# Performance work log

Measured on AMD Instinct MI355X. Metric: run time of the kernel, lower is better.

Reference implementation:

```python
import jax, jax.numpy as jnp
import numpy as np

B, N, T, FD = 128, 64, 20, 2
E, H, A = 16, 32, 32
DB, DH = 30.0, 30.0
NB, NHD = 12, 12  # 360/30 bearing and heading bins
DOMAIN_INIT = 5.0
EPS = 1e-12


def setup_inputs() -> dict:
    key = jax.random.key(0)
    ks = jax.random.split(key, 20)
    rn = lambda k, s, sc=0.1: (jax.random.normal(k, s) * sc).astype(jnp.float32)
    return {
        'x': jax.random.normal(ks[0], (B, N, T, FD), jnp.float32),
        'dmat': jax.random.uniform(ks[1], (B, N, T, N), jnp.float32) * 10.0,
        'bmat': jax.random.uniform(ks[2], (B, N, T, N), jnp.float32) * 360.0,
        'hmat': jax.random.uniform(ks[3], (B, N, T, N), jnp.float32) * 360.0,
        'mask': jnp.ones((B, N, T), jnp.float32),
        'emb_W': rn(ks[4], (E, FD)), 'emb_b': rn(ks[5], (E,)),
        'W_ih': rn(ks[6], (4 * H, E)), 'W_hh': rn(ks[7], (4 * H, H)),
        'b_ih': rn(ks[8], (4 * H,)), 'b_hh': rn(ks[9], (4 * H,)),
        'domain': jnp.full((NB, NHD), DOMAIN_INIT, jnp.float32),
        'enc2att_W': rn(ks[10], (A, H)), 'enc2att_b': rn(ks[11], (A,)),
        'spa_W': rn(ks[12], (A, 2 * A)), 'spa_b': rn(ks[13], (A,)),
        'att2enc_W': rn(ks[14], (H, A)), 'att2enc_b': rn(ks[15], (H,)),
        'cls_W': rn(ks[16], (1, H)), 'cls_b': rn(ks[17], (1,)),
        'h0': jax.random.normal(ks[18], (B * N, H), jnp.float32),
        'c0': jax.random.normal(ks[19], (B * N, H), jnp.float32),
    }


def _forward(x, dmat, bmat, hmat, mask, emb_W, emb_b, W_ih, W_hh, b_ih, b_hh,
             domain, enc2att_W, enc2att_b, spa_W, spa_b, att2enc_W, att2enc_b,
             cls_W, cls_b, h0, c0):
    # input embedding: [B,N,T,F] -> [T, B*N, E] (time-major for scan)
    xe = jnp.einsum('bntf,ef->bnte', x, emb_W) + emb_b
    xe = jnp.moveaxis(xe.reshape(B * N, T, E), 1, 0)
    dm_t = jnp.moveaxis(dmat, 2, 0)   # [T,B,N,N]
    bm_t = jnp.moveaxis(bmat, 2, 0)
    hm_t = jnp.moveaxis(hmat, 2, 0)
    mk_t = jnp.moveaxis(mask, 2, 0)   # [T,B,N]
    eye = jnp.eye(N, dtype=x.dtype)

    def step(carry, inputs):
        h, c = carry                     # [B*N, H]
        xt, dm, bm, hm, mk = inputs
        # single-step LSTM cell (torch gate order i,f,g,o)
        g = xt @ W_ih.T + b_ih + h @ W_hh.T + b_hh
        i, f, gg, o = jnp.split(g, 4, axis=-1)
        c = jax.nn.sigmoid(f) * c + jax.nn.sigmoid(i) * jnp.tanh(gg)
        h = jax.nn.sigmoid(o) * jnp.tanh(c)
        # project encoder state to attention space: [B,N,A]
        a = h.reshape(B, N, H) @ enc2att_W.T + enc2att_b
        # spatial attention weights from distance/bearing/heading edge feats
        ib = jnp.clip(jnp.floor(bm / DB), 0, NB - 1).astype(jnp.int32)
        ih = jnp.clip(jnp.floor(hm / DH), 0, NHD - 1).astype(jnp.int32)
        w = jax.nn.relu(domain[ib, ih] - dm)               # [B,N,N]
        w = w * mk[:, :, None] * mk[:, None, :] * (1.0 - eye)
        w = w / (jnp.sum(w, axis=-1, keepdims=True) + EPS)
        att = jnp.einsum('bij,bjd->bid', w, a)
        z = jnp.tanh(jnp.concatenate([a, att], axis=-1) @ spa_W.T + spa_b)
        h = (z @ att2enc_W.T + att2enc_b).reshape(B * N, H)
        return (h, c), None

    (h, c), _ = jax.lax.scan(step, (h0, c0), (xe, dm_t, bm_t, hm_t, mk_t))
    scores = jnp.tanh(h.reshape(B, N, H) @ cls_W.T + cls_b)
    return jax.nn.sigmoid(scores)  # [B, N, 1]


def reference(x, dmat, bmat, hmat, mask, emb_W, emb_b, W_ih, W_hh, b_ih, b_hh,
              domain, enc2att_W, enc2att_b, spa_W, spa_b, att2enc_W, att2enc_b,
              cls_W, cls_b, h0, c0):
    return _forward(x, dmat, bmat, hmat, mask, emb_W, emb_b, W_ih, W_hh, b_ih,
                    b_hh, domain, enc2att_W, enc2att_b, spa_W, spa_b,
                    att2enc_W, att2enc_b, cls_W, cls_b, h0, c0)
```

## Files before the change

kernel.cpp:

```cpp
#include <hip/hip_runtime.h>
#include <math.h>

#define T_STEPS 20

typedef _Float16 half8 __attribute__((ext_vector_type(8)));
typedef _Float16 half4v __attribute__((ext_vector_type(4)));
typedef float f32x4 __attribute__((ext_vector_type(4)));

__device__ __forceinline__ float sigm(float v) {
  return __builtin_amdgcn_rcpf(1.0f + __expf(-v));
}
__device__ __forceinline__ float tanh_f(float v) {
  return 1.0f - 2.0f * __builtin_amdgcn_rcpf(1.0f + __expf(2.0f * v));
}

__global__ __launch_bounds__(1024)
void traj_disc(const float* __restrict__ x, const float* __restrict__ dmat,
               const float* __restrict__ bmat, const float* __restrict__ hmat,
               const float* __restrict__ maskp,
               const float* __restrict__ embW, const float* __restrict__ embb,
               const float* __restrict__ Wih, const float* __restrict__ Whh,
               const float* __restrict__ bih, const float* __restrict__ bhh,
               const float* __restrict__ dom,
               const float* __restrict__ e2aW, const float* __restrict__ e2ab,
               const float* __restrict__ spaW, const float* __restrict__ spab,
               const float* __restrict__ a2eW, const float* __restrict__ a2eb,
               const float* __restrict__ clsW, const float* __restrict__ clsb,
               const float* __restrict__ h0p, const float* __restrict__ c0p,
               float* __restrict__ out)
{
  __shared__ __align__(16) _Float16 sgw[128*40];
  __shared__ __align__(16) _Float16 sgwc[128*40];
  __shared__ __align__(16) float4   sgmb[128];
  __shared__ __align__(16) _Float16 sESaT[32*40];
  __shared__ __align__(16) _Float16 sEStT[32*40];
  __shared__ float bz[32];
  __shared__ float sdom[144];
  __shared__ float sm[1280];
  __shared__ float sclsc[32];
  __shared__ float sclsb2[1];
  __shared__ __align__(16) _Float16 sH[64*40];
  __shared__ __align__(16) _Float16 sw[64*72];
  __shared__ __align__(16) _Float16 sz_[64*40];
  __shared__ __align__(16) _Float16 sQT[32*72];
  __shared__ __align__(16) float sgates[128*68];

  const int tid = threadIdx.x;
  const int b = blockIdx.x;
  const int i = tid >> 4;
  const int s = tid & 15;
  const int w = tid >> 6;
  const int l = tid & 63;
  const int quad = l >> 4;
  const int n16 = l & 15;

  for (int idx = tid; idx < 4096; idx += 1024) sgw[(idx >> 5)*40 + (idx & 31)] = (_Float16)Whh[idx];
  {
    const int g = tid >> 3, kb = (tid & 7) << 2;
    float a0 = 0.f, a1 = 0.f, a2 = 0.f, a3 = 0.f;
    #pragma unroll
    for (int h = 0; h < 32; ++h) {
      const float wv = Whh[g*32 + h];
      a0 = fmaf(wv, a2eW[h*32 + kb + 0], a0);
      a1 = fmaf(wv, a2eW[h*32 + kb + 1], a1);
      a2 = fmaf(wv, a2eW[h*32 + kb + 2], a2);
      a3 = fmaf(wv, a2eW[h*32 + kb + 3], a3);
    }
    sgwc[g*40 + kb + 0] = (_Float16)a0; sgwc[g*40 + kb + 1] = (_Float16)a1;
    sgwc[g*40 + kb + 2] = (_Float16)a2; sgwc[g*40 + kb + 3] = (_Float16)a3;
  }
  if (tid < 128) {
    float m0 = 0.f, m1 = 0.f, b0 = bih[tid] + bhh[tid];
    #pragma unroll
    for (int e = 0; e < 16; ++e) {
      float wv_ = Wih[tid*16 + e];
      m0 = fmaf(wv_, embW[2*e],   m0);
      m1 = fmaf(wv_, embW[2*e+1], m1);
      b0 = fmaf(wv_, embb[e],     b0);
    }
    float bn = b0;
    #pragma unroll
    for (int h = 0; h < 32; ++h) bn = fmaf(Whh[tid*32 + h], a2eb[h], bn);
    sgmb[tid] = make_float4(m0, m1, b0, bn);
  }
  {
    const int zk = tid >> 5, hc = tid & 31;
    float sa_ = 0.f, st_ = 0.f;
    #pragma unroll
    for (int a = 0; a < 32; ++a) {
      const float ev = e2aW[a*32 + hc];
      sa_ = fmaf(spaW[zk*64 + a],      ev, sa_);
      st_ = fmaf(spaW[zk*64 + 32 + a], ev, st_);
    }
    sESaT[zk*40 + hc] = (_Float16)sa_;
    sEStT[zk*40 + hc] = (_Float16)st_;
  }
  if (tid < 32) {
    float acc = spab[tid];
    #pragma unroll
    for (int a = 0; a < 32; ++a)
      acc = fmaf(e2ab[a], spaW[tid*64 + a] + spaW[tid*64 + 32 + a], acc);
    bz[tid] = acc;
    float cc = 0.f;
    #pragma unroll
    for (int h = 0; h < 32; ++h) cc = fmaf(clsW[h], a2eW[h*32 + tid], cc);
    sclsc[tid] = cc;
  }
  if (tid == 0) {
    float cb = clsb[0];
    #pragma unroll
    for (int h = 0; h < 32; ++h) cb = fmaf(clsW[h], a2eb[h], cb);
    sclsb2[0] = cb;
  }
  if (tid < 144) sdom[tid] = dom[tid];
  for (int idx = tid; idx < 1280; idx += 1024) sm[idx] = maskp[(size_t)b*1280 + idx];
  for (int idx = tid; idx < 2048; idx += 1024) sH[(idx >> 5)*40 + (idx & 31)] = (_Float16)h0p[(size_t)b*2048 + idx];
  float c0r = c0p[(size_t)b*2048 + i*32 + s];
  float c1r = c0p[(size_t)b*2048 + i*32 + s + 16];
  __syncthreads();

  const size_t nb = (size_t)b*64 + i;

  const float* xpre = x + (size_t)(b*64 + ((w >> 2) << 4) + (quad << 2)) * 40;
  float2 xA = *(const float2*)(xpre +   0);
  float2 xB = *(const float2*)(xpre +  40);
  float2 xC = *(const float2*)(xpre +  80);
  float2 xD = *(const float2*)(xpre + 120);
  size_t eb_ = nb*1280;
  float dm0 = dmat[eb_ + s],      bm0 = bmat[eb_ + s],      hm0 = hmat[eb_ + s];
  float dm1 = dmat[eb_ + s + 16], bm1 = bmat[eb_ + s + 16], hm1 = hmat[eb_ + s + 16];
  float dm2 = dmat[eb_ + s + 32], bm2 = bmat[eb_ + s + 32], hm2 = hmat[eb_ + s + 32];
  float dm3 = dmat[eb_ + s + 48], bm3 = bmat[eb_ + s + 48], hm3 = hmat[eb_ + s + 48];

  #pragma unroll 1
  for (int t = 0; t < T_STEPS; ++t) {
    {
      const int r1 = w >> 2, cp = (w & 3) << 1;
      const _Float16* Abase = (t == 0) ? sH : sz_;
      const _Float16* Bbase = (t == 0) ? sgw : sgwc;
      const half8 Af = *(const half8*)(Abase + (16*r1 + n16)*40 + quad*8);
#define OP1C(c) { \
      const half8 Bf = *(const half8*)(Bbase + (16*(c) + n16)*40 + quad*8); \
      const float4 mb = sgmb[16*(c) + n16]; \
      const float bb = (t == 0) ? mb.z : mb.w; \
      f32x4 Cv; \
      Cv[0] = fmaf(xA.x, mb.x, fmaf(xA.y, mb.y, bb)); \
      Cv[1] = fmaf(xB.x, mb.x, fmaf(xB.y, mb.y, bb)); \
      Cv[2] = fmaf(xC.x, mb.x, fmaf(xC.y, mb.y, bb)); \
      Cv[3] = fmaf(xD.x, mb.x, fmaf(xD.y, mb.y, bb)); \
      Cv = __builtin_amdgcn_mfma_f32_16x16x32_f16(Af, Bf, Cv, 0, 0, 0); \
      *(f32x4*)(sgates + (16*(c) + n16)*68 + 16*r1 + 4*quad) = Cv; }
      OP1C(cp) OP1C(cp + 1)
#undef OP1C
    }
    __syncthreads();

    {
#define GR(q, u) sgates[((q)*32 + s + 16*(u))*68 + i]
      const float ai0 = GR(0,0), af0 = GR(1,0), ag0 = GR(2,0), ao0 = GR(3,0);
      const float ai1 = GR(0,1), af1 = GR(1,1), ag1 = GR(2,1), ao1 = GR(3,1);
#undef GR
      c0r = fmaf(sigm(af0), c0r, sigm(ai0)*tanh_f(ag0));
      sH[i*40 + s]      = (_Float16)(sigm(ao0)*tanh_f(c0r));
      c1r = fmaf(sigm(af1), c1r, sigm(ai1)*tanh_f(ag1));
      sH[i*40 + s + 16] = (_Float16)(sigm(ao1)*tanh_f(c1r));
    }
    {
      const float mi_ = sm[i*20 + t];
      float rs = 0.0f;
#define WCOMP(jj) float wn##jj; { \
      int ib_ = (int)floorf(bm##jj * (1.0f/30.0f)); ib_ = ib_ < 0 ? 0 : (ib_ > 11 ? 11 : ib_); \
      int ih_ = (int)floorf(hm##jj * (1.0f/30.0f)); ih_ = ih_ < 0 ? 0 : (ih_ > 11 ? 11 : ih_); \
      float w_ = fmaxf(sdom[ib_*12 + ih_] - dm##jj, 0.0f) * (mi_ * sm[(s + 16*(jj))*20 + t]); \
      wn##jj = (s + 16*(jj) == i) ? 0.0f : w_; rs += wn##jj; }
      WCOMP(0) WCOMP(1) WCOMP(2) WCOMP(3)
#undef WCOMP
      rs += __shfl_xor(rs, 1); rs += __shfl_xor(rs, 2);
      rs += __shfl_xor(rs, 4); rs += __shfl_xor(rs, 8);
      const float inv_ = __builtin_amdgcn_rcpf(rs + 1e-12f);
      sw[i*72 + s +  0] = (_Float16)(wn0 * inv_);
      sw[i*72 + s + 16] = (_Float16)(wn1 * inv_);
      sw[i*72 + s + 32] = (_Float16)(wn2 * inv_);
      sw[i*72 + s + 48] = (_Float16)(wn3 * inv_);
    }
    {
      const int tn = (t < T_STEPS - 1) ? t + 1 : t;
      const size_t ebn = (nb*20 + tn)*64;
      dm0 = dmat[ebn + s];      bm0 = bmat[ebn + s];      hm0 = hmat[ebn + s];
      dm1 = dmat[ebn + s + 16]; bm1 = bmat[ebn + s + 16]; hm1 = hmat[ebn + s + 16];
      dm2 = dmat[ebn + s + 32]; bm2 = bmat[ebn + s + 32]; hm2 = hmat[ebn + s + 32];
      dm3 = dmat[ebn + s + 48]; bm3 = bmat[ebn + s + 48]; hm3 = hmat[ebn + s + 48];
      const int tn2 = tn << 1;
      xA = *(const float2*)(xpre + tn2);
      xB = *(const float2*)(xpre + tn2 +  40);
      xC = *(const float2*)(xpre + tn2 +  80);
      xD = *(const float2*)(xpre + tn2 + 120);
    }
    __syncthreads();

    f32x4 Pv = {0.f, 0.f, 0.f, 0.f};
    if (w < 8) {
      const int r = w >> 1, c = w & 1;
      const half8 Af = *(const half8*)(sH    + (16*r + n16)*40 + quad*8);
      const half8 Bf = *(const half8*)(sESaT + (16*c + n16)*40 + quad*8);
      const float bzv = bz[16*c + n16];
      Pv[0] = bzv; Pv[1] = bzv; Pv[2] = bzv; Pv[3] = bzv;
      Pv = __builtin_amdgcn_mfma_f32_16x16x32_f16(Af, Bf, Pv, 0, 0, 0);
    } else {
      const int w8 = w - 8, r = w8 >> 1, c = w8 & 1;
      const half8 Af = *(const half8*)(sH    + (16*r + n16)*40 + quad*8);
      const half8 Bf = *(const half8*)(sEStT + (16*c + n16)*40 + quad*8);
      f32x4 Cv = {0.f, 0.f, 0.f, 0.f};
      Cv = __builtin_amdgcn_mfma_f32_16x16x32_f16(Af, Bf, Cv, 0, 0, 0);
      half4v hq;
      hq[0] = (_Float16)Cv[0]; hq[1] = (_Float16)Cv[1];
      hq[2] = (_Float16)Cv[2]; hq[3] = (_Float16)Cv[3];
      *(half4v*)(sQT + (16*c + n16)*72 + 16*r + 4*quad) = hq;
    }
    __syncthreads();

    if (w < 8) {
      const int r = w >> 1, c = w & 1;
      const half8 A0 = *(const half8*)(sw  + (16*r + n16)*72 + quad*8);
      const half8 A1 = *(const half8*)(sw  + (16*r + n16)*72 + 32 + quad*8);
      const half8 B0 = *(const half8*)(sQT + (16*c + n16)*72 + quad*8);
      const half8 B1 = *(const half8*)(sQT + (16*c + n16)*72 + 32 + quad*8);
      Pv = __builtin_amdgcn_mfma_f32_16x16x32_f16(A0, B0, Pv, 0, 0, 0);
      Pv = __builtin_amdgcn_mfma_f32_16x16x32_f16(A1, B1, Pv, 0, 0, 0);
      const int nd = 16*r + 4*quad;
      sz_[(nd+0)*40 + 16*c + n16] = (_Float16)tanh_f(Pv[0]);
      sz_[(nd+1)*40 + 16*c + n16] = (_Float16)tanh_f(Pv[1]);
      sz_[(nd+2)*40 + 16*c + n16] = (_Float16)tanh_f(Pv[2]);
      sz_[(nd+3)*40 + 16*c + n16] = (_Float16)tanh_f(Pv[3]);
    }
    __syncthreads();
  }

  if (tid < 64) {
    float acc = sclsb2[0];
    #pragma unroll
    for (int k = 0; k < 32; ++k) acc = fmaf((float)sz_[tid*40 + k], sclsc[k], acc);
    out[(size_t)b*64 + tid] = sigm(tanh_f(acc));
  }
}

extern "C" void kernel_launch(void* const* d_in, const int* in_sizes, int n_in,
                              void* d_out, int out_size, void* d_ws, size_t ws_size,
                              hipStream_t stream) {
  (void)in_sizes; (void)n_in; (void)d_ws; (void)ws_size; (void)out_size;
  const float* x    = (const float*)d_in[0];
  const float* dmat = (const float*)d_in[1];
  const float* bmat = (const float*)d_in[2];
  const float* hmat = (const float*)d_in[3];
  const float* mask = (const float*)d_in[4];
  const float* embW = (const float*)d_in[5];
  const float* embb = (const float*)d_in[6];
  const float* Wih  = (const float*)d_in[7];
  const float* Whh  = (const float*)d_in[8];
  const float* bih  = (const float*)d_in[9];
  const float* bhh  = (const float*)d_in[10];
  const float* dom  = (const float*)d_in[11];
  const float* e2aW = (const float*)d_in[12];
  const float* e2ab = (const float*)d_in[13];
  const float* spaW = (const float*)d_in[14];
  const float* spab = (const float*)d_in[15];
  const float* a2eW = (const float*)d_in[16];
  const float* a2eb = (const float*)d_in[17];
  const float* clsW = (const float*)d_in[18];
  const float* clsb = (const float*)d_in[19];
  const float* h0   = (const float*)d_in[20];
  const float* c0   = (const float*)d_in[21];
  float* out = (float*)d_out;

  traj_disc<<<dim3(128), dim3(1024), 0, stream>>>(
      x, dmat, bmat, hmat, mask, embW, embb, Wih, Whh, bih, bhh, dom,
      e2aW, e2ab, spaW, spab, a2eW, a2eb, clsW, clsb, h0, c0, out);
}
```

Measured before the change: 225.0 us.

## Specialize waves into LSTM and attention-weight groups and drop two barriers per step

Waves 0-7 now compute all eight gate tiles for their row block, apply the LSTM nonlinearities directly on the MFMA accumulators, and recompute the full Q projection each. Waves 8-15 take over the edge-weight computation and the dmat/bmat/hmat prefetch, with 8 edges per thread. This removes the sgates LDS round trip and cuts the barriers per timestep from four to two. The cost is that each of waves 0-7 repeats the Q MFMA work, several waves write identical sQT values, and register pressure per thread goes up.

After: 239.9 us. 1.07x slower.

```diff
diff --git a/kernel.cpp b/kernel.cpp
--- a/kernel.cpp
+++ b/kernel.cpp
@@ -4,7 +4,6 @@
 #define T_STEPS 20
 
 typedef _Float16 half8 __attribute__((ext_vector_type(8)));
-typedef _Float16 half4v __attribute__((ext_vector_type(4)));
 typedef float f32x4 __attribute__((ext_vector_type(4)));
 
 __device__ __forceinline__ float sigm(float v) {
@@ -40,15 +39,12 @@
   __shared__ float sclsc[32];
   __shared__ float sclsb2[1];
   __shared__ __align__(16) _Float16 sH[64*40];
-  __shared__ __align__(16) _Float16 sw[64*72];
+  __shared__ __align__(16) _Float16 sw_[64*72];
   __shared__ __align__(16) _Float16 sz_[64*40];
   __shared__ __align__(16) _Float16 sQT[32*72];
-  __shared__ __align__(16) float sgates[128*68];
 
   const int tid = threadIdx.x;
   const int b = blockIdx.x;
-  const int i = tid >> 4;
-  const int s = tid & 15;
   const int w = tid >> 6;
   const int l = tid & 63;
   const int quad = l >> 4;
@@ -115,32 +111,57 @@
   if (tid < 144) sdom[tid] = dom[tid];
   for (int idx = tid; idx < 1280; idx += 1024) sm[idx] = maskp[(size_t)b*1280 + idx];
   for (int idx = tid; idx < 2048; idx += 1024) sH[(idx >> 5)*40 + (idx & 31)] = (_Float16)h0p[(size_t)b*2048 + idx];
-  float c0r = c0p[(size_t)b*2048 + i*32 + s];
-  float c1r = c0p[(size_t)b*2048 + i*32 + s + 16];
   __syncthreads();
 
-  const size_t nb = (size_t)b*64 + i;
-
-  const float* xpre = x + (size_t)(b*64 + ((w >> 2) << 4) + (quad << 2)) * 40;
-  float2 xA = *(const float2*)(xpre +   0);
-  float2 xB = *(const float2*)(xpre +  40);
-  float2 xC = *(const float2*)(xpre +  80);
-  float2 xD = *(const float2*)(xpre + 120);
-  size_t eb_ = nb*1280;
-  float dm0 = dmat[eb_ + s],      bm0 = bmat[eb_ + s],      hm0 = hmat[eb_ + s];
-  float dm1 = dmat[eb_ + s + 16], bm1 = bmat[eb_ + s + 16], hm1 = hmat[eb_ + s + 16];
-  float dm2 = dmat[eb_ + s + 32], bm2 = bmat[eb_ + s + 32], hm2 = hmat[eb_ + s + 32];
-  float dm3 = dmat[eb_ + s + 48], bm3 = bmat[eb_ + s + 48], hm3 = hmat[eb_ + s + 48];
+  int r = 0, csel = 0;
+  half8 EA = {0}, ET = {0};
+  float bzv = 0.f;
+  const float* xpre = x;
+  float2 xA = {0,0}, xB = {0,0}, xC = {0,0}, xD = {0,0};
+  float cA0=0, cA1=0, cA2=0, cA3=0, cB0=0, cB1=0, cB2=0, cB3=0;
+  int i3 = 0, s8 = 0;
+  float dm0=0,dm1=0,dm2=0,dm3=0,dm4=0,dm5=0,dm6=0,dm7=0;
+  float bm0=0,bm1=0,bm2=0,bm3=0,bm4=0,bm5=0,bm6=0,bm7=0;
+  float hm0=0,hm1=0,hm2=0,hm3=0,hm4=0,hm5=0,hm6=0,hm7=0;
+
+  if (w < 8) {
+    r = w >> 1; csel = w & 1;
+    EA = *(const half8*)(sESaT + (16*csel + n16)*40 + quad*8);
+    ET = *(const half8*)(sEStT + (16*csel + n16)*40 + quad*8);
+    bzv = bz[16*csel + n16];
+    xpre = x + (size_t)(b*64 + 16*r + 4*quad) * 40;
+    xA = *(const float2*)(xpre +   0);
+    xB = *(const float2*)(xpre +  40);
+    xC = *(const float2*)(xpre +  80);
+    xD = *(const float2*)(xpre + 120);
+    const size_t cb0 = (size_t)(b*64 + 16*r + 4*quad)*32 + n16;
+    cA0 = c0p[cb0];        cA1 = c0p[cb0 + 32];
+    cA2 = c0p[cb0 + 64];   cA3 = c0p[cb0 + 96];
+    cB0 = c0p[cb0 + 16];   cB1 = c0p[cb0 + 48];
+    cB2 = c0p[cb0 + 80];   cB3 = c0p[cb0 + 112];
+  } else {
+    const int t8 = tid - 512;
+    i3 = t8 >> 3; s8 = t8 & 7;
+    const size_t eb0 = ((size_t)(b*64 + i3)*20 + 0)*64 + s8;
+    dm0 = dmat[eb0];      bm0 = bmat[eb0];      hm0 = hmat[eb0];
+    dm1 = dmat[eb0 +  8]; bm1 = bmat[eb0 +  8]; hm1 = hmat[eb0 +  8];
+    dm2 = dmat[eb0 + 16]; bm2 = bmat[eb0 + 16]; hm2 = hmat[eb0 + 16];
+    dm3 = dmat[eb0 + 24]; bm3 = bmat[eb0 + 24]; hm3 = hmat[eb0 + 24];
+    dm4 = dmat[eb0 + 32]; bm4 = bmat[eb0 + 32]; hm4 = hmat[eb0 + 32];
+    dm5 = dmat[eb0 + 40]; bm5 = bmat[eb0 + 40]; hm5 = hmat[eb0 + 40];
+    dm6 = dmat[eb0 + 48]; bm6 = bmat[eb0 + 48]; hm6 = hmat[eb0 + 48];
+    dm7 = dmat[eb0 + 56]; bm7 = bmat[eb0 + 56]; hm7 = hmat[eb0 + 56];
+  }
 
   #pragma unroll 1
   for (int t = 0; t < T_STEPS; ++t) {
-    {
-      const int r1 = w >> 2, cp = (w & 3) << 1;
-      const _Float16* Abase = (t == 0) ? sH : sz_;
-      const _Float16* Bbase = (t == 0) ? sgw : sgwc;
-      const half8 Af = *(const half8*)(Abase + (16*r1 + n16)*40 + quad*8);
-#define OP1C(c) { \
-      const half8 Bf = *(const half8*)(Bbase + (16*(c) + n16)*40 + quad*8); \
+    if (w < 8) {
+      const _Float16* Ab = (t == 0) ? sH : sz_;
+      const _Float16* Bb = (t == 0) ? sgw : sgwc;
+      const half8 Af = *(const half8*)(Ab + (16*r + n16)*40 + quad*8);
+      f32x4 G0, G1, G2, G3, G4, G5, G6, G7;
+#define OP1C(c, Gd) { \
+      const half8 Bf = *(const half8*)(Bb + (16*(c) + n16)*40 + quad*8); \
       const float4 mb = sgmb[16*(c) + n16]; \
       const float bb = (t == 0) ? mb.z : mb.w; \
       f32x4 Cv; \
@@ -148,90 +169,86 @@
       Cv[1] = fmaf(xB.x, mb.x, fmaf(xB.y, mb.y, bb)); \
       Cv[2] = fmaf(xC.x, mb.x, fmaf(xC.y, mb.y, bb)); \
       Cv[3] = fmaf(xD.x, mb.x, fmaf(xD.y, mb.y, bb)); \
-      Cv = __builtin_amdgcn_mfma_f32_16x16x32_f16(Af, Bf, Cv, 0, 0, 0); \
-      *(f32x4*)(sgates + (16*(c) + n16)*68 + 16*r1 + 4*quad) = Cv; }
-      OP1C(cp) OP1C(cp + 1)
+      Gd = __builtin_amdgcn_mfma_f32_16x16x32_f16(Af, Bf, Cv, 0, 0, 0); }
+      OP1C(0, G0) OP1C(1, G1) OP1C(2, G2) OP1C(3, G3)
+      OP1C(4, G4) OP1C(5, G5) OP1C(6, G6) OP1C(7, G7)
 #undef OP1C
-    }
-    __syncthreads();
-
-    {
-#define GR(q, u) sgates[((q)*32 + s + 16*(u))*68 + i]
-      const float ai0 = GR(0,0), af0 = GR(1,0), ag0 = GR(2,0), ao0 = GR(3,0);
-      const float ai1 = GR(0,1), af1 = GR(1,1), ag1 = GR(2,1), ao1 = GR(3,1);
-#undef GR
-      c0r = fmaf(sigm(af0), c0r, sigm(ai0)*tanh_f(ag0));
-      sH[i*40 + s]      = (_Float16)(sigm(ao0)*tanh_f(c0r));
-      c1r = fmaf(sigm(af1), c1r, sigm(ai1)*tanh_f(ag1));
-      sH[i*40 + s + 16] = (_Float16)(sigm(ao1)*tanh_f(c1r));
-    }
-    {
-      const float mi_ = sm[i*20 + t];
+#define NL(Gi, Gf, Gg, Go, k, creg, hho) { \
+      const float ii = sigm(Gi[k]), ff = sigm(Gf[k]); \
+      const float gg = tanh_f(Gg[k]), oo = sigm(Go[k]); \
+      creg = fmaf(ff, creg, ii*gg); \
+      sH[(16*r + 4*quad + (k))*40 + n16 + (hho)] = (_Float16)(oo * tanh_f(creg)); }
+      NL(G0, G2, G4, G6, 0, cA0, 0)  NL(G0, G2, G4, G6, 1, cA1, 0)
+      NL(G0, G2, G4, G6, 2, cA2, 0)  NL(G0, G2, G4, G6, 3, cA3, 0)
+      NL(G1, G3, G5, G7, 0, cB0, 16) NL(G1, G3, G5, G7, 1, cB1, 16)
+      NL(G1, G3, G5, G7, 2, cB2, 16) NL(G1, G3, G5, G7, 3, cB3, 16)
+#undef NL
+    } else {
+      const float mi_ = sm[i3*20 + t];
       float rs = 0.0f;
 #define WCOMP(jj) float wn##jj; { \
       int ib_ = (int)floorf(bm##jj * (1.0f/30.0f)); ib_ = ib_ < 0 ? 0 : (ib_ > 11 ? 11 : ib_); \
       int ih_ = (int)floorf(hm##jj * (1.0f/30.0f)); ih_ = ih_ < 0 ? 0 : (ih_ > 11 ? 11 : ih_); \
-      float w_ = fmaxf(sdom[ib_*12 + ih_] - dm##jj, 0.0f) * (mi_ * sm[(s + 16*(jj))*20 + t]); \
-      wn##jj = (s + 16*(jj) == i) ? 0.0f : w_; rs += wn##jj; }
-      WCOMP(0) WCOMP(1) WCOMP(2) WCOMP(3)
+      float w_ = fmaxf(sdom[ib_*12 + ih_] - dm##jj, 0.0f) * (mi_ * sm[(s8 + 8*(jj))*20 + t]); \
+      wn##jj = (s8 + 8*(jj) == i3) ? 0.0f : w_; rs += wn##jj; }
+      WCOMP(0) WCOMP(1) WCOMP(2) WCOMP(3) WCOMP(4) WCOMP(5) WCOMP(6) WCOMP(7)
 #undef WCOMP
-      rs += __shfl_xor(rs, 1); rs += __shfl_xor(rs, 2);
-      rs += __shfl_xor(rs, 4); rs += __shfl_xor(rs, 8);
+      rs += __shfl_xor(rs, 1); rs += __shfl_xor(rs, 2); rs += __shfl_xor(rs, 4);
       const float inv_ = __builtin_amdgcn_rcpf(rs + 1e-12f);
-      sw[i*72 + s +  0] = (_Float16)(wn0 * inv_);
-      sw[i*72 + s + 16] = (_Float16)(wn1 * inv_);
-      sw[i*72 + s + 32] = (_Float16)(wn2 * inv_);
-      sw[i*72 + s + 48] = (_Float16)(wn3 * inv_);
-    }
-    {
-      const int tn = (t < T_STEPS - 1) ? t + 1 : t;
-      const size_t ebn = (nb*20 + tn)*64;
-      dm0 = dmat[ebn + s];      bm0 = bmat[ebn + s];      hm0 = hmat[ebn + s];
-      dm1 = dmat[ebn + s + 16]; bm1 = bmat[ebn + s + 16]; hm1 = hmat[ebn + s + 16];
-      dm2 = dmat[ebn + s + 32]; bm2 = bmat[ebn + s + 32]; hm2 = hmat[ebn + s + 32];
-      dm3 = dmat[ebn + s + 48]; bm3 = bmat[ebn + s + 48]; hm3 = hmat[ebn + s + 48];
-      const int tn2 = tn << 1;
+      sw_[i3*72 + s8 +  0] = (_Float16)(wn0 * inv_);
+      sw_[i3*72 + s8 +  8] = (_Float16)(wn1 * inv_);
+      sw_[i3*72 + s8 + 16] = (_Float16)(wn2 * inv_);
+      sw_[i3*72 + s8 + 24] = (_Float16)(wn3 * inv_);
+      sw_[i3*72 + s8 + 32] = (_Float16)(wn4 * inv_);
+      sw_[i3*72 + s8 + 40] = (_Float16)(wn5 * inv_);
+      sw_[i3*72 + s8 + 48] = (_Float16)(wn6 * inv_);
+      sw_[i3*72 + s8 + 56] = (_Float16)(wn7 * inv_);
+    }
+    __syncthreads();
+
+    if (w < 8) {
+      const half8 Hr0 = *(const half8*)(sH + (      n16)*40 + quad*8);
+      const half8 Hr1 = *(const half8*)(sH + (16  + n16)*40 + quad*8);
+      const half8 Hr2 = *(const half8*)(sH + (32  + n16)*40 + quad*8);
+      const half8 Hr3 = *(const half8*)(sH + (48  + n16)*40 + quad*8);
+      const half8 HrR = (r == 0) ? Hr0 : (r == 1) ? Hr1 : (r == 2) ? Hr2 : Hr3;
+      f32x4 Pv = {bzv, bzv, bzv, bzv};
+      Pv = __builtin_amdgcn_mfma_f32_16x16x32_f16(HrR, EA, Pv, 0, 0, 0);
+#define QT(rq, Afr) { \
+      f32x4 Qv = {0.f, 0.f, 0.f, 0.f}; \
+      Qv = __builtin_amdgcn_mfma_f32_16x16x32_f16(Afr, ET, Qv, 0, 0, 0); \
+      _Float16* qd = sQT + (16*csel + n16)*72 + 16*(rq) + 4*quad; \
+      qd[0] = (_Float16)Qv[0]; qd[1] = (_Float16)Qv[1]; \
+      qd[2] = (_Float16)Qv[2]; qd[3] = (_Float16)Qv[3]; }
+      QT(0, Hr0) QT(1, Hr1) QT(2, Hr2) QT(3, Hr3)
+#undef QT
+      const half8 A0 = *(const half8*)(sw_ + (16*r + n16)*72 + quad*8);
+      const half8 A1 = *(const half8*)(sw_ + (16*r + n16)*72 + 32 + quad*8);
+      const half8 B0 = *(const half8*)(sQT + (16*csel + n16)*72 + quad*8);
+      const half8 B1 = *(const half8*)(sQT + (16*csel + n16)*72 + 32 + quad*8);
+      Pv = __builtin_amdgcn_mfma_f32_16x16x32_f16(A0, B0, Pv, 0, 0, 0);
+      Pv = __builtin_amdgcn_mfma_f32_16x16x32_f16(A1, B1, Pv, 0, 0, 0);
+      _Float16* zd = sz_ + (16*r + 4*quad)*40 + 16*csel + n16;
+      zd[0]   = (_Float16)tanh_f(Pv[0]);
+      zd[40]  = (_Float16)tanh_f(Pv[1]);
+      zd[80]  = (_Float16)tanh_f(Pv[2]);
+      zd[120] = (_Float16)tanh_f(Pv[3]);
+      const int tn2 = ((t < T_STEPS - 1) ? t + 1 : t) << 1;
       xA = *(const float2*)(xpre + tn2);
       xB = *(const float2*)(xpre + tn2 +  40);
       xC = *(const float2*)(xpre + tn2 +  80);
       xD = *(const float2*)(xpre + tn2 + 120);
-    }
-    __syncthreads();
-
-    f32x4 Pv = {0.f, 0.f, 0.f, 0.f};
-    if (w < 8) {
-      const int r = w >> 1, c = w & 1;
-      const half8 Af = *(const half8*)(sH    + (16*r + n16)*40 + quad*8);
-      const half8 Bf = *(const half8*)(sESaT + (16*c + n16)*40 + quad*8);
-      const float bzv = bz[16*c + n16];
-      Pv[0] = bzv; Pv[1] = bzv; Pv[2] = bzv; Pv[3] = bzv;
-      Pv = __builtin_amdgcn_mfma_f32_16x16x32_f16(Af, Bf, Pv, 0, 0, 0);
     } else {
-      const int w8 = w - 8, r = w8 >> 1, c = w8 & 1;
-      const half8 Af = *(const half8*)(sH    + (16*r + n16)*40 + quad*8);
-      const half8 Bf = *(const half8*)(sEStT + (16*c + n16)*40 + quad*8);
-      f32x4 Cv = {0.f, 0.f, 0.f, 0.f};
-      Cv = __builtin_amdgcn_mfma_f32_16x16x32_f16(Af, Bf, Cv, 0, 0, 0);
-      half4v hq;
-      hq[0] = (_Float16)Cv[0]; hq[1] = (_Float16)Cv[1];
-      hq[2] = (_Float16)Cv[2]; hq[3] = (_Float16)Cv[3];
-      *(half4v*)(sQT + (16*c + n16)*72 + 16*r + 4*quad) = hq;
-    }
-    __syncthreads();
-
-    if (w < 8) {
-      const int r = w >> 1, c = w & 1;
-      const half8 A0 = *(const half8*)(sw  + (16*r + n16)*72 + quad*8);
-      const half8 A1 = *(const half8*)(sw  + (16*r + n16)*72 + 32 + quad*8);
-      const half8 B0 = *(const half8*)(sQT + (16*c + n16)*72 + quad*8);
-      const half8 B1 = *(const half8*)(sQT + (16*c + n16)*72 + 32 + quad*8);
-      Pv = __builtin_amdgcn_mfma_f32_16x16x32_f16(A0, B0, Pv, 0, 0, 0);
-      Pv = __builtin_amdgcn_mfma_f32_16x16x32_f16(A1, B1, Pv, 0, 0, 0);
-      const int nd = 16*r + 4*quad;
-      sz_[(nd+0)*40 + 16*c + n16] = (_Float16)tanh_f(Pv[0]);
-      sz_[(nd+1)*40 + 16*c + n16] = (_Float16)tanh_f(Pv[1]);
-      sz_[(nd+2)*40 + 16*c + n16] = (_Float16)tanh_f(Pv[2]);
-      sz_[(nd+3)*40 + 16*c + n16] = (_Float16)tanh_f(Pv[3]);
+      const int tn = (t < T_STEPS - 1) ? t + 1 : t;
+      const size_t ebn = ((size_t)(b*64 + i3)*20 + tn)*64 + s8;
+      dm0 = dmat[ebn];      bm0 = bmat[ebn];      hm0 = hmat[ebn];
+      dm1 = dmat[ebn +  8]; bm1 = bmat[ebn +  8]; hm1 = hmat[ebn +  8];
+      dm2 = dmat[ebn + 16]; bm2 = bmat[ebn + 16]; hm2 = hmat[ebn + 16];
+      dm3 = dmat[ebn + 24]; bm3 = bmat[ebn + 24]; hm3 = hmat[ebn + 24];
+      dm4 = dmat[ebn + 32]; bm4 = bmat[ebn + 32]; hm4 = hmat[ebn + 32];
+      dm5 = dmat[ebn + 40]; bm5 = bmat[ebn + 40]; hm5 = hmat[ebn + 40];
+      dm6 = dmat[ebn + 48]; bm6 = bmat[ebn + 48]; hm6 = hmat[ebn + 48];
+      dm7 = dmat[ebn + 56]; bm7 = bmat[ebn + 56]; hm7 = hmat[ebn + 56];
     }
     __syncthreads();
   }
```

## Precompute normalized attention weights in a parallel prep kernel before recurrence

Applied to the files above, without the earlier changes.

Moves the per-timestep edge-weight computation (domain lookup, relu, masking, row normalization) out of the serial 20-step recurrence into a separate fully parallel kernel that writes fp16 weights to workspace. The main kernel then loads the weight fragments straight into MFMA operand registers, prefetching the next step's fragments. It also hoists the constant spatial-projection B fragments into registers. This takes the weight math off the critical path and drops one sync per step, at the cost of an extra launch and an fp16 round-trip through global memory. A fallback path keeps the old fused kernel when the workspace is too small.

After: 238.0 us. 5.8% more time.

```diff
diff --git a/kernel.cpp b/kernel.cpp
--- a/kernel.cpp
+++ b/kernel.cpp
@@ -14,20 +14,270 @@
   return 1.0f - 2.0f * __builtin_amdgcn_rcpf(1.0f + __expf(2.0f * v));
 }
 
+__global__ __launch_bounds__(256)
+void prep_w(const float* __restrict__ dmat, const float* __restrict__ bmat,
+            const float* __restrict__ hmat, const float* __restrict__ maskp,
+            const float* __restrict__ dom, _Float16* __restrict__ wout)
+{
+  __shared__ float sdom[144];
+  __shared__ float smk[64];
+  const int tid = threadIdx.x;
+  const int bt = blockIdx.x;
+  const int b = bt / 20, t = bt - b*20;
+  if (tid < 144) sdom[tid] = dom[tid];
+  if (tid < 64) smk[tid] = maskp[(size_t)b*1280 + tid*20 + t];
+  __syncthreads();
+  const int i  = tid >> 2;
+  const int jb = (tid & 3) << 4;
+  const size_t eb = ((size_t)(b*64 + i)*20 + t)*64 + jb;
+  const float mi = smk[i];
+  float rs = 0.f;
+#define WC(k) float wv##k; { \
+  const float dmv = dmat[eb + (k)]; \
+  const float bmv = bmat[eb + (k)]; \
+  const float hmv = hmat[eb + (k)]; \
+  int ib_ = (int)floorf(bmv * (1.0f/30.0f)); ib_ = ib_ < 0 ? 0 : (ib_ > 11 ? 11 : ib_); \
+  int ih_ = (int)floorf(hmv * (1.0f/30.0f)); ih_ = ih_ < 0 ? 0 : (ih_ > 11 ? 11 : ih_); \
+  float w_ = fmaxf(sdom[ib_*12 + ih_] - dmv, 0.0f) * (mi * smk[jb + (k)]); \
+  wv##k = (jb + (k) == i) ? 0.0f : w_; rs += wv##k; }
+  WC(0) WC(1) WC(2) WC(3) WC(4) WC(5) WC(6) WC(7)
+  WC(8) WC(9) WC(10) WC(11) WC(12) WC(13) WC(14) WC(15)
+#undef WC
+  rs += __shfl_xor(rs, 1); rs += __shfl_xor(rs, 2);
+  const float inv = __builtin_amdgcn_rcpf(rs + 1e-12f);
+  half8 o0, o1;
+  o0[0]=(_Float16)(wv0*inv);  o0[1]=(_Float16)(wv1*inv);
+  o0[2]=(_Float16)(wv2*inv);  o0[3]=(_Float16)(wv3*inv);
+  o0[4]=(_Float16)(wv4*inv);  o0[5]=(_Float16)(wv5*inv);
+  o0[6]=(_Float16)(wv6*inv);  o0[7]=(_Float16)(wv7*inv);
+  o1[0]=(_Float16)(wv8*inv);  o1[1]=(_Float16)(wv9*inv);
+  o1[2]=(_Float16)(wv10*inv); o1[3]=(_Float16)(wv11*inv);
+  o1[4]=(_Float16)(wv12*inv); o1[5]=(_Float16)(wv13*inv);
+  o1[6]=(_Float16)(wv14*inv); o1[7]=(_Float16)(wv15*inv);
+  _Float16* dst = wout + ((size_t)bt*64 + i)*64 + jb;
+  *(half8*)(dst)     = o0;
+  *(half8*)(dst + 8) = o1;
+}
+
 __global__ __launch_bounds__(1024)
-void traj_disc(const float* __restrict__ x, const float* __restrict__ dmat,
-               const float* __restrict__ bmat, const float* __restrict__ hmat,
-               const float* __restrict__ maskp,
-               const float* __restrict__ embW, const float* __restrict__ embb,
-               const float* __restrict__ Wih, const float* __restrict__ Whh,
-               const float* __restrict__ bih, const float* __restrict__ bhh,
-               const float* __restrict__ dom,
-               const float* __restrict__ e2aW, const float* __restrict__ e2ab,
-               const float* __restrict__ spaW, const float* __restrict__ spab,
-               const float* __restrict__ a2eW, const float* __restrict__ a2eb,
-               const float* __restrict__ clsW, const float* __restrict__ clsb,
-               const float* __restrict__ h0p, const float* __restrict__ c0p,
-               float* __restrict__ out)
+void traj_disc_main(const float* __restrict__ x,
+                    const float* __restrict__ embW, const float* __restrict__ embb,
+                    const float* __restrict__ Wih, const float* __restrict__ Whh,
+                    const float* __restrict__ bih, const float* __restrict__ bhh,
+                    const float* __restrict__ e2aW, const float* __restrict__ e2ab,
+                    const float* __restrict__ spaW, const float* __restrict__ spab,
+                    const float* __restrict__ a2eW, const float* __restrict__ a2eb,
+                    const float* __restrict__ clsW, const float* __restrict__ clsb,
+                    const float* __restrict__ h0p, const float* __restrict__ c0p,
+                    const _Float16* __restrict__ wglob,
+                    float* __restrict__ out)
+{
+  __shared__ __align__(16) _Float16 sgw[128*40];
+  __shared__ __align__(16) _Float16 sgwc[128*40];
+  __shared__ __align__(16) float4   sgmb[128];
+  __shared__ __align__(16) _Float16 sESaT[32*40];
+  __shared__ __align__(16) _Float16 sEStT[32*40];
+  __shared__ float bz[32];
+  __shared__ float sclsc[32];
+  __shared__ float sclsb2[1];
+  __shared__ __align__(16) _Float16 sH[64*40];
+  __shared__ __align__(16) _Float16 sz_[64*40];
+  __shared__ __align__(16) _Float16 sQT[32*72];
+  __shared__ __align__(16) float sgates[128*68];
+
+  const int tid = threadIdx.x;
+  const int b = blockIdx.x;
+  const int i = tid >> 4;
+  const int s = tid & 15;
+  const int w = tid >> 6;
+  const int l = tid & 63;
+  const int quad = l >> 4;
+  const int n16 = l & 15;
+
+  for (int idx = tid; idx < 4096; idx += 1024) sgw[(idx >> 5)*40 + (idx & 31)] = (_Float16)Whh[idx];
+  {
+    const int g = tid >> 3, kb = (tid & 7) << 2;
+    float a0 = 0.f, a1 = 0.f, a2 = 0.f, a3 = 0.f;
+    #pragma unroll
+    for (int h = 0; h < 32; ++h) {
+      const float wv = Whh[g*32 + h];
+      a0 = fmaf(wv, a2eW[h*32 + kb + 0], a0);
+      a1 = fmaf(wv, a2eW[h*32 + kb + 1], a1);
+      a2 = fmaf(wv, a2eW[h*32 + kb + 2], a2);
+      a3 = fmaf(wv, a2eW[h*32 + kb + 3], a3);
+    }
+    sgwc[g*40 + kb + 0] = (_Float16)a0; sgwc[g*40 + kb + 1] = (_Float16)a1;
+    sgwc[g*40 + kb + 2] = (_Float16)a2; sgwc[g*40 + kb + 3] = (_Float16)a3;
+  }
+  if (tid < 128) {
+    float m0 = 0.f, m1 = 0.f, b0 = bih[tid] + bhh[tid];
+    #pragma unroll
+    for (int e = 0; e < 16; ++e) {
+      float wv_ = Wih[tid*16 + e];
+      m0 = fmaf(wv_, embW[2*e],   m0);
+      m1 = fmaf(wv_, embW[2*e+1], m1);
+      b0 = fmaf(wv_, embb[e],     b0);
+    }
+    float bn = b0;
+    #pragma unroll
+    for (int h = 0; h < 32; ++h) bn = fmaf(Whh[tid*32 + h], a2eb[h], bn);
+    sgmb[tid] = make_float4(m0, m1, b0, bn);
+  }
+  {
+    const int zk = tid >> 5, hc = tid & 31;
+    float sa_ = 0.f, st_ = 0.f;
+    #pragma unroll
+    for (int a = 0; a < 32; ++a) {
+      const float ev = e2aW[a*32 + hc];
+      sa_ = fmaf(spaW[zk*64 + a],      ev, sa_);
+      st_ = fmaf(spaW[zk*64 + 32 + a], ev, st_);
+    }
+    sESaT[zk*40 + hc] = (_Float16)sa_;
+    sEStT[zk*40 + hc] = (_Float16)st_;
+  }
+  if (tid < 32) {
+    float acc = spab[tid];
+    #pragma unroll
+    for (int a = 0; a < 32; ++a)
+      acc = fmaf(e2ab[a], spaW[tid*64 + a] + spaW[tid*64 + 32 + a], acc);
+    bz[tid] = acc;
+    float cc = 0.f;
+    #pragma unroll
+    for (int h = 0; h < 32; ++h) cc = fmaf(clsW[h], a2eW[h*32 + tid], cc);
+    sclsc[tid] = cc;
+  }
+  if (tid == 0) {
+    float cb = clsb[0];
+    #pragma unroll
+    for (int h = 0; h < 32; ++h) cb = fmaf(clsW[h], a2eb[h], cb);
+    sclsb2[0] = cb;
+  }
+  for (int idx = tid; idx < 2048; idx += 1024) sH[(idx >> 5)*40 + (idx & 31)] = (_Float16)h0p[(size_t)b*2048 + idx];
+  float c0r = c0p[(size_t)b*2048 + i*32 + s];
+  float c1r = c0p[(size_t)b*2048 + i*32 + s + 16];
+  __syncthreads();
+
+  const float* xpre = x + (size_t)(b*64 + ((w >> 2) << 4) + (quad << 2)) * 40;
+  float2 xA = *(const float2*)(xpre +   0);
+  float2 xB = *(const float2*)(xpre +  40);
+  float2 xC = *(const float2*)(xpre +  80);
+  float2 xD = *(const float2*)(xpre + 120);
+  half8 Bconst;
+  float bzv = 0.f;
+  half8 wA0 = {0}, wA1 = {0};
+  if (w < 8) {
+    const int c = w & 1, r = w >> 1;
+    Bconst = *(const half8*)(sESaT + (16*c + n16)*40 + quad*8);
+    bzv = bz[16*c + n16];
+    const _Float16* wp = wglob + ((size_t)(b*20 + 0)*64 + 16*r + n16)*64 + quad*8;
+    wA0 = *(const half8*)(wp);
+    wA1 = *(const half8*)(wp + 32);
+  } else {
+    const int c = (w - 8) & 1;
+    Bconst = *(const half8*)(sEStT + (16*c + n16)*40 + quad*8);
+  }
+
+  #pragma unroll 1
+  for (int t = 0; t < T_STEPS; ++t) {
+    {
+      const int r1 = w >> 2, cp = (w & 3) << 1;
+      const _Float16* Ab = (t == 0) ? sH : sz_;
+      const _Float16* Bb = (t == 0) ? sgw : sgwc;
+      const half8 Af = *(const half8*)(Ab + (16*r1 + n16)*40 + quad*8);
+#define OP1C(c) { \
+      const half8 Bf = *(const half8*)(Bb + (16*(c) + n16)*40 + quad*8); \
+      const float4 mb = sgmb[16*(c) + n16]; \
+      const float bb = (t == 0) ? mb.z : mb.w; \
+      f32x4 Cv; \
+      Cv[0] = fmaf(xA.x, mb.x, fmaf(xA.y, mb.y, bb)); \
+      Cv[1] = fmaf(xB.x, mb.x, fmaf(xB.y, mb.y, bb)); \
+      Cv[2] = fmaf(xC.x, mb.x, fmaf(xC.y, mb.y, bb)); \
+      Cv[3] = fmaf(xD.x, mb.x, fmaf(xD.y, mb.y, bb)); \
+      Cv = __builtin_amdgcn_mfma_f32_16x16x32_f16(Af, Bf, Cv, 0, 0, 0); \
+      *(f32x4*)(sgates + (16*(c) + n16)*68 + 16*r1 + 4*quad) = Cv; }
+      OP1C(cp) OP1C(cp + 1)
+#undef OP1C
+    }
+    {
+      const int tn2 = ((t < T_STEPS - 1) ? t + 1 : t) << 1;
+      xA = *(const float2*)(xpre + tn2);
+      xB = *(const float2*)(xpre + tn2 +  40);
+      xC = *(const float2*)(xpre + tn2 +  80);
+      xD = *(const float2*)(xpre + tn2 + 120);
+    }
+    __syncthreads();
+
+    {
+#define GR(q, u) sgates[((q)*32 + s + 16*(u))*68 + i]
+      const float ai0 = GR(0,0), af0 = GR(1,0), ag0 = GR(2,0), ao0 = GR(3,0);
+      const float ai1 = GR(0,1), af1 = GR(1,1), ag1 = GR(2,1), ao1 = GR(3,1);
+#undef GR
+      c0r = fmaf(sigm(af0), c0r, sigm(ai0)*tanh_f(ag0));
+      sH[i*40 + s]      = (_Float16)(sigm(ao0)*tanh_f(c0r));
+      c1r = fmaf(sigm(af1), c1r, sigm(ai1)*tanh_f(ag1));
+      sH[i*40 + s + 16] = (_Float16)(sigm(ao1)*tanh_f(c1r));
+    }
+    __syncthreads();
+
+    f32x4 Pv = {0.f, 0.f, 0.f, 0.f};
+    if (w < 8) {
+      const int r = w >> 1;
+      const half8 Af = *(const half8*)(sH + (16*r + n16)*40 + quad*8);
+      Pv[0] = bzv; Pv[1] = bzv; Pv[2] = bzv; Pv[3] = bzv;
+      Pv = __builtin_amdgcn_mfma_f32_16x16x32_f16(Af, Bconst, Pv, 0, 0, 0);
+    } else {
+      const int w8 = w - 8, r = w8 >> 1, c = w8 & 1;
+      const half8 Af = *(const half8*)(sH + (16*r + n16)*40 + quad*8);
+      f32x4 Cv = {0.f, 0.f, 0.f, 0.f};
+      Cv = __builtin_amdgcn_mfma_f32_16x16x32_f16(Af, Bconst, Cv, 0, 0, 0);
+      half4v hq;
+      hq[0] = (_Float16)Cv[0]; hq[1] = (_Float16)Cv[1];
+      hq[2] = (_Float16)Cv[2]; hq[3] = (_Float16)Cv[3];
+      *(half4v*)(sQT + (16*c + n16)*72 + 16*r + 4*quad) = hq;
+    }
+    __syncthreads();
+
+    if (w < 8) {
+      const int r = w >> 1, c = w & 1;
+      const half8 B0 = *(const half8*)(sQT + (16*c + n16)*72 + quad*8);
+      const half8 B1 = *(const half8*)(sQT + (16*c + n16)*72 + 32 + quad*8);
+      Pv = __builtin_amdgcn_mfma_f32_16x16x32_f16(wA0, B0, Pv, 0, 0, 0);
+      Pv = __builtin_amdgcn_mfma_f32_16x16x32_f16(wA1, B1, Pv, 0, 0, 0);
+      _Float16* zd = sz_ + (16*r + 4*quad)*40 + 16*c + n16;
+      zd[0]   = (_Float16)tanh_f(Pv[0]);
+      zd[40]  = (_Float16)tanh_f(Pv[1]);
+      zd[80]  = (_Float16)tanh_f(Pv[2]);
+      zd[120] = (_Float16)tanh_f(Pv[3]);
+      const int tn = (t < T_STEPS - 1) ? t + 1 : t;
+      const _Float16* wp = wglob + ((size_t)(b*20 + tn)*64 + 16*r + n16)*64 + quad*8;
+      wA0 = *(const half8*)(wp);
+      wA1 = *(const half8*)(wp + 32);
+    }
+    __syncthreads();
+  }
+
+  if (tid < 64) {
+    float acc = sclsb2[0];
+    #pragma unroll
+    for (int k = 0; k < 32; ++k) acc = fmaf((float)sz_[tid*40 + k], sclsc[k], acc);
+    out[(size_t)b*64 + tid] = sigm(tanh_f(acc));
+  }
+}
+
+__global__ __launch_bounds__(1024)
+void traj_disc_fb(const float* __restrict__ x, const float* __restrict__ dmat,
+                  const float* __restrict__ bmat, const float* __restrict__ hmat,
+                  const float* __restrict__ maskp,
+                  const float* __restrict__ embW, const float* __restrict__ embb,
+                  const float* __restrict__ Wih, const float* __restrict__ Whh,
+                  const float* __restrict__ bih, const float* __restrict__ bhh,
+                  const float* __restrict__ dom,
+                  const float* __restrict__ e2aW, const float* __restrict__ e2ab,
+                  const float* __restrict__ spaW, const float* __restrict__ spab,
+                  const float* __restrict__ a2eW, const float* __restrict__ a2eb,
+                  const float* __restrict__ clsW, const float* __restrict__ clsb,
+                  const float* __restrict__ h0p, const float* __restrict__ c0p,
+                  float* __restrict__ out)
 {
   __shared__ __align__(16) _Float16 sgw[128*40];
   __shared__ __align__(16) _Float16 sgwc[128*40];
@@ -40,7 +290,7 @@
   __shared__ float sclsc[32];
   __shared__ float sclsb2[1];
   __shared__ __align__(16) _Float16 sH[64*40];
-  __shared__ __align__(16) _Float16 sw[64*72];
+  __shared__ __align__(16) _Float16 sw_[64*72];
   __shared__ __align__(16) _Float16 sz_[64*40];
   __shared__ __align__(16) _Float16 sQT[32*72];
   __shared__ __align__(16) float sgates[128*68];
@@ -120,7 +370,6 @@
   __syncthreads();
 
   const size_t nb = (size_t)b*64 + i;
-
   const float* xpre = x + (size_t)(b*64 + ((w >> 2) << 4) + (quad << 2)) * 40;
   float2 xA = *(const float2*)(xpre +   0);
   float2 xB = *(const float2*)(xpre +  40);
@@ -136,11 +385,11 @@
   for (int t = 0; t < T_STEPS; ++t) {
     {
       const int r1 = w >> 2, cp = (w & 3) << 1;
-      const _Float16* Abase = (t == 0) ? sH : sz_;
-      const _Float16* Bbase = (t == 0) ? sgw : sgwc;
-      const half8 Af = *(const half8*)(Abase + (16*r1 + n16)*40 + quad*8);
+      const _Float16* Ab = (t == 0) ? sH : sz_;
+      const _Float16* Bb = (t == 0) ? sgw : sgwc;
+      const half8 Af = *(const half8*)(Ab + (16*r1 + n16)*40 + quad*8);
 #define OP1C(c) { \
-      const half8 Bf = *(const half8*)(Bbase + (16*(c) + n16)*40 + quad*8); \
+      const half8 Bf = *(const half8*)(Bb + (16*(c) + n16)*40 + quad*8); \
       const float4 mb = sgmb[16*(c) + n16]; \
       const float bb = (t == 0) ? mb.z : mb.w; \
       f32x4 Cv; \
@@ -154,7 +403,6 @@
 #undef OP1C
     }
     __syncthreads();
-
     {
 #define GR(q, u) sgates[((q)*32 + s + 16*(u))*68 + i]
       const float ai0 = GR(0,0), af0 = GR(1,0), ag0 = GR(2,0), ao0 = GR(3,0);
@@ -178,10 +426,10 @@
       rs += __shfl_xor(rs, 1); rs += __shfl_xor(rs, 2);
       rs += __shfl_xor(rs, 4); rs += __shfl_xor(rs, 8);
       const float inv_ = __builtin_amdgcn_rcpf(rs + 1e-12f);
-      sw[i*72 + s +  0] = (_Float16)(wn0 * inv_);
-      sw[i*72 + s + 16] = (_Float16)(wn1 * inv_);
-      sw[i*72 + s + 32] = (_Float16)(wn2 * inv_);
-      sw[i*72 + s + 48] = (_Float16)(wn3 * inv_);
+      sw_[i*72 + s +  0] = (_Float16)(wn0 * inv_);
+      sw_[i*72 + s + 16] = (_Float16)(wn1 * inv_);
+      sw_[i*72 + s + 32] = (_Float16)(wn2 * inv_);
+      sw_[i*72 + s + 48] = (_Float16)(wn3 * inv_);
     }
     {
       const int tn = (t < T_STEPS - 1) ? t + 1 : t;
@@ -197,7 +445,6 @@
       xD = *(const float2*)(xpre + tn2 + 120);
     }
     __syncthreads();
-
     f32x4 Pv = {0.f, 0.f, 0.f, 0.f};
     if (w < 8) {
       const int r = w >> 1, c = w & 1;
@@ -218,20 +465,19 @@
       *(half4v*)(sQT + (16*c + n16)*72 + 16*r + 4*quad) = hq;
     }
     __syncthreads();
-
     if (w < 8) {
       const int r = w >> 1, c = w & 1;
-      const half8 A0 = *(const half8*)(sw  + (16*r + n16)*72 + quad*8);
-      const half8 A1 = *(const half8*)(sw  + (16*r + n16)*72 + 32 + quad*8);
+      const half8 A0 = *(const half8*)(sw_ + (16*r + n16)*72 + quad*8);
+      const half8 A1 = *(const half8*)(sw_ + (16*r + n16)*72 + 32 + quad*8);
       const half8 B0 = *(const half8*)(sQT + (16*c + n16)*72 + quad*8);
       const half8 B1 = *(const half8*)(sQT + (16*c + n16)*72 + 32 + quad*8);
       Pv = __builtin_amdgcn_mfma_f32_16x16x32_f16(A0, B0, Pv, 0, 0, 0);
       Pv = __builtin_amdgcn_mfma_f32_16x16x32_f16(A1, B1, Pv, 0, 0, 0);
-      const int nd = 16*r + 4*quad;
-      sz_[(nd+0)*40 + 16*c + n16] = (_Float16)tanh_f(Pv[0]);
-      sz_[(nd+1)*40 + 16*c + n16] = (_Float16)tanh_f(Pv[1]);
-      sz_[(nd+2)*40 + 16*c + n16] = (_Float16)tanh_f(Pv[2]);
-      sz_[(nd+3)*40 + 16*c + n16] = (_Float16)tanh_f(Pv[3]);
+      _Float16* zd = sz_ + (16*r + 4*quad)*40 + 16*c + n16;
+      zd[0]   = (_Float16)tanh_f(Pv[0]);
+      zd[40]  = (_Float16)tanh_f(Pv[1]);
+      zd[80]  = (_Float16)tanh_f(Pv[2]);
+      zd[120] = (_Float16)tanh_f(Pv[3]);
     }
     __syncthreads();
   }
@@ -247,7 +493,7 @@
 extern "C" void kernel_launch(void* const* d_in, const int* in_sizes, int n_in,
                               void* d_out, int out_size, void* d_ws, size_t ws_size,
                               hipStream_t stream) {
-  (void)in_sizes; (void)n_in; (void)d_ws; (void)ws_size; (void)out_size;
+  (void)in_sizes; (void)n_in; (void)out_size;
   const float* x    = (const float*)d_in[0];
   const float* dmat = (const float*)d_in[1];
   const float* bmat = (const float*)d_in[2];
@@ -272,7 +518,16 @@
   const float* c0   = (const float*)d_in[21];
   float* out = (float*)d_out;
 
-  traj_disc<<<dim3(128), dim3(1024), 0, stream>>>(
-      x, dmat, bmat, hmat, mask, embW, embb, Wih, Whh, bih, bhh, dom,
-      e2aW, e2ab, spaW, spab, a2eW, a2eb, clsW, clsb, h0, c0, out);
+  const size_t WNEED = (size_t)128 * 20 * 64 * 64 * sizeof(_Float16);
+  if (ws_size >= WNEED) {
+    _Float16* wbuf = (_Float16*)d_ws;
+    prep_w<<<dim3(128*20), dim3(256), 0, stream>>>(dmat, bmat, hmat, mask, dom, wbuf);
+    traj_disc_main<<<dim3(128), dim3(1024), 0, stream>>>(
+        x, embW, embb, Wih, Whh, bih, bhh, e2aW, e2ab, spaW, spab,
+        a2eW, a2eb, clsW, clsb, h0, c0, wbuf, out);
+  } else {
+    traj_disc_fb<<<dim3(128), dim3(1024), 0, stream>>>(
+        x, dmat, bmat, hmat, mask, embW, embb, Wih, Whh, bih, bhh, dom,
+        e2aW, e2ab, spaW, spab, a2eW, a2eb, clsW, clsb, h0, c0, out);
+  }
 }
```
